# Optimization experiments

Measured on AMD Instinct MI355X. Metric: run time of the kernel, lower is better.

Reference implementation:

```python
import jax, jax.numpy as jnp
import numpy as np

FP32_MIN = jnp.float32(-3.402823e+38)


def setup_inputs() -> dict:
    key = jax.random.key(0)
    k1, k2 = jax.random.split(key)
    B, E, D, N = 8, 50000, 128, 10000
    data = jax.random.normal(k1, (B, E, D), dtype=jnp.float32)
    indices = jax.random.randint(k2, (B, E), 0, N, dtype=jnp.int32)
    beta = jnp.ones((), dtype=jnp.float32)  # trainable weight, initializer='ones'
    return {"data": data, "beta": beta, "indices": indices, "num_segments": N}


def reference(data, beta, indices, num_segments):
    # aggregators = ['sum','max','mean','var','softmax'] -> concat order:
    #   sum | max | [mean, relu(var)] (fused mean_and_var, stable_var=True) | softmax
    def per_batch(d, idx):
        # d: [E, D], idx: [E]
        ssum = jax.ops.segment_sum(d, idx, num_segments=num_segments)          # [N, D]
        smax = jax.ops.segment_max(d, idx, num_segments=num_segments)          # [N, D]
        smax = jnp.where(smax <= FP32_MIN, jnp.float32(0), smax)               # empty segments -> 0
        ones = jnp.ones((d.shape[0], 1), dtype=d.dtype)
        counts = jax.ops.segment_sum(ones, idx, num_segments=num_segments)     # [N, 1]
        counts_c = jnp.maximum(counts, jnp.float32(1))
        mean = ssum / counts_c                                                 # [N, D]
        # stable var: center by per-graph feature mean before scattering
        d_mean = jnp.mean(d, axis=0, keepdims=True)                            # [1, D]
        var = jax.ops.segment_sum((d - d_mean) * (d - d_mean), idx,
                                  num_segments=num_segments) / counts_c        # [N, D]
        var = jax.nn.relu(var)
        # scatter softmax (global max-shift for stability; constant per graph)
        d_t = d - jnp.max(d)
        num = jnp.exp(beta * d_t)                                              # [E, D]
        denom = jax.ops.segment_sum(num, idx, num_segments=num_segments)       # [N, D]
        denom_g = denom[idx]                                                   # gather back: [E, D]
        denom_g = jnp.where(denom_g != 0, denom_g, jnp.float32(1))
        soft = jax.ops.segment_sum(d * (num / denom_g), idx,
                                   num_segments=num_segments)                  # [N, D]
        return jnp.concatenate([ssum, smax, mean, var, soft], axis=-1)         # [N, 5D]

    return jax.vmap(per_batch)(data, indices)  # [B, N, 5D]
```

## Files before the change

kernel.cpp:

```cpp
#include <hip/hip_runtime.h>

#define B 8
#define E 50000
#define D 128
#define NSEG 10000
#define OUTD (5 * D)

#define FLT_MAX_F 3.402823466e+38f


__global__ void hist_kernel(const int* __restrict__ idx, int* __restrict__ counts) {
    int t = blockIdx.x * 256 + threadIdx.x;
    if (t >= B * E) return;
    int b = t / E;
    atomicAdd(&counts[b * NSEG + idx[t]], 1);
}

__global__ void scan_kernel(const int* __restrict__ counts, int* __restrict__ offsets,
                            int* __restrict__ cursor) {
    int b = blockIdx.x;
    __shared__ int wsum[16];
    __shared__ int s_carry;
    if (threadIdx.x == 0) s_carry = 0;
    __syncthreads();
    int wid = threadIdx.x >> 6;
    int lane = threadIdx.x & 63;
    for (int base = 0; base < NSEG; base += 1024) {
        int i = base + threadIdx.x;
        int v = (i < NSEG) ? counts[b * NSEG + i] : 0;
        int x = v;
        #pragma unroll
        for (int off = 1; off < 64; off <<= 1) {
            int t = __shfl_up(x, off, 64);
            if (lane >= off) x += t;
        }
        if (lane == 63) wsum[wid] = x;
        __syncthreads();
        int carry = s_carry;
        __syncthreads();
        if (threadIdx.x == 0) {
            int acc = 0;
            #pragma unroll
            for (int k = 0; k < 16; ++k) { int t = wsum[k]; wsum[k] = acc; acc += t; }
            s_carry = carry + acc;
        }
        __syncthreads();
        int excl = carry + wsum[wid] + x - v;
        if (i < NSEG) {
            offsets[b * NSEG + i] = excl;
            cursor[b * NSEG + i] = excl;
        }
        __syncthreads();
    }
}

__global__ void scatter_kernel(const int* __restrict__ idx, int* __restrict__ cursor,
                               int* __restrict__ perm) {
    int t = blockIdx.x * 256 + threadIdx.x;
    if (t >= B * E) return;
    int b = t / E;
    int e = t - b * E;
    int pos = atomicAdd(&cursor[b * NSEG + idx[t]], 1);
    perm[b * E + pos] = e;
}

__global__ void agg_kernel(const float* __restrict__ data, const float* __restrict__ beta_p,
                           const int* __restrict__ counts, const int* __restrict__ offsets,
                           const int* __restrict__ perm, float* __restrict__ out) {
    int w = (blockIdx.x * 256 + threadIdx.x) >> 6;
    int lane = threadIdx.x & 63;
    if (w >= B * NSEG) return;
    int b = w / NSEG;
    int cnt = counts[w];
    int off = offsets[w];
    float beta = *beta_p;

    float s0 = 0.f, s1 = 0.f;
    float q0 = 0.f, q1 = 0.f;
    float m0 = -FLT_MAX_F, m1 = -FLT_MAX_F;
    float es0 = 0.f, es1 = 0.f;
    float ws0 = 0.f, ws1 = 0.f;

    const int* pp = perm + b * E + off;
    const float* dbase = data + (size_t)b * E * D;
    for (int j = 0; j < cnt; ++j) {
        int e = pp[j];
        float2 v = ((const float2*)(dbase + (size_t)e * D))[lane];
        s0 += v.x; s1 += v.y;
        q0 = fmaf(v.x, v.x, q0); q1 = fmaf(v.y, v.y, q1);
        m0 = fmaxf(m0, v.x); m1 = fmaxf(m1, v.y);
        float ex0 = expf(beta * v.x);
        float ex1 = expf(beta * v.y);
        es0 += ex0; es1 += ex1;
        ws0 = fmaf(v.x, ex0, ws0); ws1 = fmaf(v.y, ex1, ws1);
    }

    float cc = fmaxf((float)cnt, 1.0f);
    float mean0 = s0 / cc, mean1 = s1 / cc;
    float mx0 = cnt ? m0 : 0.f, mx1 = cnt ? m1 : 0.f;
    float sf0 = cnt ? ws0 / es0 : 0.f, sf1 = cnt ? ws1 / es1 : 0.f;

    float* o = out + (size_t)w * OUTD;
    ((float2*)(o        ))[lane] = make_float2(s0, s1);
    ((float2*)(o +     D))[lane] = make_float2(mx0, mx1);
    ((float2*)(o + 2 * D))[lane] = make_float2(mean0, mean1);
    ((float2*)(o + 3 * D))[lane] = make_float2(q0, q1);
    ((float2*)(o + 4 * D))[lane] = make_float2(sf0, sf1);
}

#define K5_CHUNK 100
__global__ void colsum_kernel(const float* __restrict__ out, float* __restrict__ colsum) {
    int chunks = NSEG / K5_CHUNK;
    int b = blockIdx.x / chunks;
    int n0 = (blockIdx.x % chunks) * K5_CHUNK;
    int d = threadIdx.x & 127;
    int half = threadIdx.x >> 7;
    float partial = 0.f;
    for (int r = half; r < K5_CHUNK; r += 2) {
        partial += out[(size_t)(b * NSEG + n0 + r) * OUTD + d];
    }
    atomicAdd(&colsum[b * D + d], partial);
}

__global__ void var_kernel(const float* __restrict__ colsum, const int* __restrict__ counts,
                           float* __restrict__ out) {
    int t = blockIdx.x * 256 + threadIdx.x;
    if (t >= B * NSEG * 64) return;
    int w = t >> 6;
    int lane = t & 63;
    int b = w / NSEG;
    int cnt = counts[w];
    float c = (float)cnt;
    float cc = fmaxf(c, 1.0f);
    float frac = c / cc;
    float* o = out + (size_t)w * OUTD;
    float2 q = ((const float2*)(o + 3 * D))[lane];
    float2 mn = ((const float2*)(o + 2 * D))[lane];
    const float invE = 1.0f / (float)E;
    float dm0 = colsum[b * D + 2 * lane] * invE;
    float dm1 = colsum[b * D + 2 * lane + 1] * invE;
    float v0 = q.x / cc - 2.f * dm0 * mn.x + frac * dm0 * dm0;
    float v1 = q.y / cc - 2.f * dm1 * mn.y + frac * dm1 * dm1;
    ((float2*)(o + 3 * D))[lane] = make_float2(fmaxf(v0, 0.f), fmaxf(v1, 0.f));
}

extern "C" void kernel_launch(void* const* d_in, const int* in_sizes, int n_in,
                              void* d_out, int out_size, void* d_ws, size_t ws_size,
                              hipStream_t stream) {
    const float* data = (const float*)d_in[0];
    const float* beta = (const float*)d_in[1];
    const int* indices = (const int*)d_in[2];
    float* out = (float*)d_out;

    int* counts   = (int*)d_ws;
    float* colsum = (float*)d_ws + 80000;
    int* offsets  = (int*)d_ws + 81024;
    int* cursor   = (int*)d_ws + 161024;
    int* perm     = (int*)d_ws + 241024;

    hipMemsetAsync(d_ws, 0, (size_t)(80000 + 1024) * 4, stream);

    hist_kernel<<<(B * E + 255) / 256, 256, 0, stream>>>(indices, counts);
    scan_kernel<<<B, 1024, 0, stream>>>(counts, offsets, cursor);
    scatter_kernel<<<(B * E + 255) / 256, 256, 0, stream>>>(indices, cursor, perm);
    agg_kernel<<<(B * NSEG * 64) / 256, 256, 0, stream>>>(data, beta, counts, offsets, perm, out);
    colsum_kernel<<<B * (NSEG / K5_CHUNK), 256, 0, stream>>>(out, colsum);
    var_kernel<<<(B * NSEG * 64) / 256, 256, 0, stream>>>(colsum, counts, out);
}
```

Measured before the change: 479.7 us.

## Fuse column-sum into histogram pass and variance finalization into aggregation

Computes per-batch column sums directly from the input data inside the histogram kernel. The variance finalization moves into the aggregation kernel, which removes the separate colsum and var kernels and their extra read/write passes over the output. The aggregation loop now loads the segment's indices cooperatively, broadcasts them with shuffles, and issues 8 row loads before computing, which raises memory-level parallelism. It also uses exp2 with a prescaled beta and drops the offsets array by deriving each offset from the post-scatter cursor. The cost is an extra full read of the data in the histogram pass.

```diff
diff --git a/kernel.cpp b/kernel.cpp
--- a/kernel.cpp
+++ b/kernel.cpp
@@ -7,17 +7,41 @@
 #define OUTD (5 * D)
 
 #define FLT_MAX_F 3.402823466e+38f
+#define LOG2E 1.4426950408889634f
 
 
-__global__ void hist_kernel(const int* __restrict__ idx, int* __restrict__ counts) {
-    int t = blockIdx.x * 256 + threadIdx.x;
-    if (t >= B * E) return;
-    int b = t / E;
-    atomicAdd(&counts[b * NSEG + idx[t]], 1);
+#define HC_BLOCKS_PER_B 128
+__global__ void hist_colsum_kernel(const float* __restrict__ data, const int* __restrict__ idx,
+                                   int* __restrict__ counts, float* __restrict__ colsum) {
+    int b = blockIdx.x / HC_BLOCKS_PER_B;
+    int chunk = blockIdx.x % HC_BLOCKS_PER_B;
+    const int per = (E + HC_BLOCKS_PER_B - 1) / HC_BLOCKS_PER_B;
+    int r0 = chunk * per;
+    int r1 = min(E, r0 + per);
+
+    for (int r = r0 + (int)threadIdx.x; r < r1; r += 256)
+        atomicAdd(&counts[b * NSEG + idx[b * E + r]], 1);
+
+    int wid = threadIdx.x >> 6, lane = threadIdx.x & 63;
+    float c0 = 0.f, c1 = 0.f;
+    const float* dbase = data + (size_t)b * E * D;
+    for (int r = r0 + wid; r < r1; r += 4) {
+        float2 v = ((const float2*)(dbase + (size_t)r * D))[lane];
+        c0 += v.x; c1 += v.y;
+    }
+    __shared__ float red[4][128];
+    red[wid][2 * lane] = c0;
+    red[wid][2 * lane + 1] = c1;
+    __syncthreads();
+    if (wid == 0) {
+        float t0 = red[0][2 * lane] + red[1][2 * lane] + red[2][2 * lane] + red[3][2 * lane];
+        float t1 = red[0][2 * lane + 1] + red[1][2 * lane + 1] + red[2][2 * lane + 1] + red[3][2 * lane + 1];
+        atomicAdd(&colsum[b * D + 2 * lane], t0);
+        atomicAdd(&colsum[b * D + 2 * lane + 1], t1);
+    }
 }
 
-__global__ void scan_kernel(const int* __restrict__ counts, int* __restrict__ offsets,
-                            int* __restrict__ cursor) {
+__global__ void scan_kernel(const int* __restrict__ counts, int* __restrict__ cursor) {
     int b = blockIdx.x;
     __shared__ int wsum[16];
     __shared__ int s_carry;
@@ -46,10 +70,7 @@
         }
         __syncthreads();
         int excl = carry + wsum[wid] + x - v;
-        if (i < NSEG) {
-            offsets[b * NSEG + i] = excl;
-            cursor[b * NSEG + i] = excl;
-        }
+        if (i < NSEG) cursor[b * NSEG + i] = excl;
         __syncthreads();
     }
 }
@@ -64,16 +85,18 @@
     perm[b * E + pos] = e;
 }
 
-__global__ void agg_kernel(const float* __restrict__ data, const float* __restrict__ beta_p,
-                           const int* __restrict__ counts, const int* __restrict__ offsets,
-                           const int* __restrict__ perm, float* __restrict__ out) {
+__global__ __launch_bounds__(256) void agg_kernel(
+        const float* __restrict__ data, const float* __restrict__ beta_p,
+        const int* __restrict__ counts, const int* __restrict__ cursor,
+        const int* __restrict__ perm, const float* __restrict__ colsum,
+        float* __restrict__ out) {
     int w = (blockIdx.x * 256 + threadIdx.x) >> 6;
     int lane = threadIdx.x & 63;
     if (w >= B * NSEG) return;
     int b = w / NSEG;
     int cnt = counts[w];
-    int off = offsets[w];
-    float beta = *beta_p;
+    int off = cursor[w] - cnt;
+    float k2 = beta_p[0] * LOG2E;
 
     float s0 = 0.f, s1 = 0.f;
     float q0 = 0.f, q1 = 0.f;
@@ -83,65 +106,57 @@
 
     const int* pp = perm + b * E + off;
     const float* dbase = data + (size_t)b * E * D;
-    for (int j = 0; j < cnt; ++j) {
-        int e = pp[j];
-        float2 v = ((const float2*)(dbase + (size_t)e * D))[lane];
-        s0 += v.x; s1 += v.y;
-        q0 = fmaf(v.x, v.x, q0); q1 = fmaf(v.y, v.y, q1);
-        m0 = fmaxf(m0, v.x); m1 = fmaxf(m1, v.y);
-        float ex0 = expf(beta * v.x);
-        float ex1 = expf(beta * v.y);
-        es0 += ex0; es1 += ex1;
-        ws0 = fmaf(v.x, ex0, ws0); ws1 = fmaf(v.y, ex1, ws1);
+
+    for (int base = 0; base < cnt; base += 64) {
+        int rem = cnt - base;
+        int m = rem < 64 ? rem : 64;
+        int el = (lane < m) ? pp[base + lane] : 0;
+        for (int j0 = 0; j0 < m; j0 += 8) {
+            float2 v[8];
+            #pragma unroll
+            for (int k = 0; k < 8; ++k) {
+                int j = j0 + k;
+                if (j < m) {
+                    int ej = __shfl(el, j, 64);
+                    v[k] = ((const float2*)(dbase + (size_t)ej * D))[lane];
+                }
+            }
+            #pragma unroll
+            for (int k = 0; k < 8; ++k) {
+                if (j0 + k < m) {
+                    float2 x = v[k];
+                    s0 += x.x; s1 += x.y;
+                    q0 = fmaf(x.x, x.x, q0); q1 = fmaf(x.y, x.y, q1);
+                    m0 = fmaxf(m0, x.x); m1 = fmaxf(m1, x.y);
+                    float e0 = __builtin_amdgcn_exp2f(k2 * x.x);
+                    float e1 = __builtin_amdgcn_exp2f(k2 * x.y);
+                    es0 += e0; es1 += e1;
+                    ws0 = fmaf(x.x, e0, ws0); ws1 = fmaf(x.y, e1, ws1);
+                }
+            }
+        }
     }
 
-    float cc = fmaxf((float)cnt, 1.0f);
-    float mean0 = s0 / cc, mean1 = s1 / cc;
+    float c = (float)cnt;
+    float cc = fmaxf(c, 1.0f);
+    float inv = 1.0f / cc;
+    float mean0 = s0 * inv, mean1 = s1 * inv;
     float mx0 = cnt ? m0 : 0.f, mx1 = cnt ? m1 : 0.f;
     float sf0 = cnt ? ws0 / es0 : 0.f, sf1 = cnt ? ws1 / es1 : 0.f;
+
+    const float invE = 1.0f / (float)E;
+    float dm0 = colsum[b * D + 2 * lane] * invE;
+    float dm1 = colsum[b * D + 2 * lane + 1] * invE;
+    float frac = c * inv;
+    float v0 = fmaxf(q0 * inv - 2.f * dm0 * mean0 + frac * dm0 * dm0, 0.f);
+    float v1 = fmaxf(q1 * inv - 2.f * dm1 * mean1 + frac * dm1 * dm1, 0.f);
 
     float* o = out + (size_t)w * OUTD;
     ((float2*)(o        ))[lane] = make_float2(s0, s1);
     ((float2*)(o +     D))[lane] = make_float2(mx0, mx1);
     ((float2*)(o + 2 * D))[lane] = make_float2(mean0, mean1);
-    ((float2*)(o + 3 * D))[lane] = make_float2(q0, q1);
+    ((float2*)(o + 3 * D))[lane] = make_float2(v0, v1);
     ((float2*)(o + 4 * D))[lane] = make_float2(sf0, sf1);
-}
-
-#define K5_CHUNK 100
-__global__ void colsum_kernel(const float* __restrict__ out, float* __restrict__ colsum) {
-    int chunks = NSEG / K5_CHUNK;
-    int b = blockIdx.x / chunks;
-    int n0 = (blockIdx.x % chunks) * K5_CHUNK;
-    int d = threadIdx.x & 127;
-    int half = threadIdx.x >> 7;
-    float partial = 0.f;
-    for (int r = half; r < K5_CHUNK; r += 2) {
-        partial += out[(size_t)(b * NSEG + n0 + r) * OUTD + d];
-    }
-    atomicAdd(&colsum[b * D + d], partial);
-}
-
-__global__ void var_kernel(const float* __restrict__ colsum, const int* __restrict__ counts,
-                           float* __restrict__ out) {
-    int t = blockIdx.x * 256 + threadIdx.x;
-    if (t >= B * NSEG * 64) return;
-    int w = t >> 6;
-    int lane = t & 63;
-    int b = w / NSEG;
-    int cnt = counts[w];
-    float c = (float)cnt;
-    float cc = fmaxf(c, 1.0f);
-    float frac = c / cc;
-    float* o = out + (size_t)w * OUTD;
-    float2 q = ((const float2*)(o + 3 * D))[lane];
-    float2 mn = ((const float2*)(o + 2 * D))[lane];
-    const float invE = 1.0f / (float)E;
-    float dm0 = colsum[b * D + 2 * lane] * invE;
-    float dm1 = colsum[b * D + 2 * lane + 1] * invE;
-    float v0 = q.x / cc - 2.f * dm0 * mn.x + frac * dm0 * dm0;
-    float v1 = q.y / cc - 2.f * dm1 * mn.y + frac * dm1 * dm1;
-    ((float2*)(o + 3 * D))[lane] = make_float2(fmaxf(v0, 0.f), fmaxf(v1, 0.f));
 }
 
 extern "C" void kernel_launch(void* const* d_in, const int* in_sizes, int n_in,
@@ -154,16 +169,14 @@
 
     int* counts   = (int*)d_ws;
     float* colsum = (float*)d_ws + 80000;
-    int* offsets  = (int*)d_ws + 81024;
-    int* cursor   = (int*)d_ws + 161024;
-    int* perm     = (int*)d_ws + 241024;
+    int* cursor   = (int*)d_ws + 81024;
+    int* perm     = (int*)d_ws + 161024;
 
     hipMemsetAsync(d_ws, 0, (size_t)(80000 + 1024) * 4, stream);
 
-    hist_kernel<<<(B * E + 255) / 256, 256, 0, stream>>>(indices, counts);
-    scan_kernel<<<B, 1024, 0, stream>>>(counts, offsets, cursor);
+    hist_colsum_kernel<<<B * HC_BLOCKS_PER_B, 256, 0, stream>>>(data, indices, counts, colsum);
+    scan_kernel<<<B, 1024, 0, stream>>>(counts, cursor);
     scatter_kernel<<<(B * E + 255) / 256, 256, 0, stream>>>(indices, cursor, perm);
-    agg_kernel<<<(B * NSEG * 64) / 256, 256, 0, stream>>>(data, beta, counts, offsets, perm, out);
-    colsum_kernel<<<B * (NSEG / K5_CHUNK), 256, 0, stream>>>(out, colsum);
-    var_kernel<<<(B * NSEG * 64) / 256, 256, 0, stream>>>(colsum, counts, out);
+    agg_kernel<<<(B * NSEG * 64) / 256, 256, 0, stream>>>(data, beta, counts, cursor, perm,
+                                                          colsum, out);
 }
```

New measurement: 455.8 us. 1.05x faster.
